# Performance work log

Measured on AMD Instinct MI355X. Metric: run time of the kernel, lower is better.

The kernel has to match this reference:

```python
import jax, jax.numpy as jnp
import numpy as np

HEADS = 8
DIM_HEAD = 64
WINDOW = 512
SCALE = DIM_HEAD ** -0.5


def setup_inputs() -> dict:
    key = jax.random.key(0)
    k1, k2, k3 = jax.random.split(key, 3)
    b, dim, n = 2, 256, 32768
    hidden = HEADS * DIM_HEAD  # 512
    x = jax.random.normal(k1, (b, dim, n), dtype=jnp.float32)
    # Conv1d(dim, hidden*3, 1, bias=False) weight -> [3*hidden, dim]
    w_qkv = jax.random.normal(k2, (3 * hidden, dim), dtype=jnp.float32) * (dim ** -0.5)
    # Conv1d(hidden, dim, 1) weight/bias
    w_out = jax.random.normal(k3, (dim, hidden), dtype=jnp.float32) * (hidden ** -0.5)
    b_out = jnp.zeros((dim,), dtype=jnp.float32)
    return {"x": x, "w_qkv": w_qkv, "w_out": w_out, "b_out": b_out}


def reference(x, w_qkv, w_out, b_out):
    b, c, n = x.shape
    h, d, w = HEADS, DIM_HEAD, WINDOW
    nw = n // w  # n chosen divisible by window size
    # 1x1 conv == channel matmul
    qkv = jnp.einsum('oc,bcn->bon', w_qkv, x)  # [b, 3*h*d, n]
    q, k, v = jnp.split(qkv, 3, axis=1)
    # [b, h, d, nw, w]
    def to_windows(t):
        return t.reshape(b, h, d, nw, w)
    q = to_windows(q) * SCALE
    k = to_windows(k)
    v = to_windows(v)
    # non-overlapping local windows: block-diagonal attention
    sim = jnp.einsum('bhdni,bhdnj->bhnij', q, k)        # [b,h,nw,w,w]
    attn = jax.nn.softmax(sim, axis=-1)
    out = jnp.einsum('bhnij,bhdnj->bhdni', attn, v)      # [b,h,d,nw,w]
    out = out.reshape(b, h * d, n)
    return jnp.einsum('oc,bcn->bon', w_out, out) + b_out[None, :, None]
```

## Files before the change

### kernel.cpp

```cpp
#include <hip/hip_runtime.h>
#include <stdint.h>
#include <stddef.h>


typedef _Float16 f16;
typedef _Float16 half8 __attribute__((ext_vector_type(8)));
typedef float f32x4 __attribute__((ext_vector_type(4)));

#define NSEQ 32768
#define NTOT 65536
#define WIN  512

__device__ __forceinline__ void async_copy16(const f16* g, f16* l) {
  __builtin_amdgcn_global_load_lds(
      (const __attribute__((address_space(1))) void*)g,
      (__attribute__((address_space(3))) void*)l, 16, 0, 0);
}

__device__ __forceinline__ int packrtz(float a, float b) {
  typedef __fp16 fp16v2 __attribute__((ext_vector_type(2)));
  fp16v2 h = __builtin_amdgcn_cvt_pkrtz(a, b);
  return __builtin_bit_cast(int, h);
}

__global__ __launch_bounds__(256) void convert_w(
    const float* __restrict__ wqkv, const float* __restrict__ wout,
    f16* __restrict__ wqh, f16* __restrict__ woh) {
  int idx = blockIdx.x * 256 + threadIdx.x;
  if (idx < 1536 * 256) {
    float v = wqkv[idx];
    if (idx < 512 * 256) v *= 0.125f;
    wqh[idx] = (f16)v;
  } else {
    int j = idx - 1536 * 256;
    if (j < 256 * 512) woh[j] = (f16)wout[j];
  }
}

__global__ __launch_bounds__(256) void transpose_x(
    const float* __restrict__ x, f16* __restrict__ xT) {
  __shared__ alignas(16) float tile[32][33];
  const int tx = threadIdx.x & 31, ty = threadIdx.x >> 5;
  const int bx = blockIdx.x, by = blockIdx.y;
  const float* xb = x + (size_t)blockIdx.z * 256 * NSEQ;
  f16* xTb = xT + (size_t)blockIdx.z * NSEQ * 256;
#pragma unroll
  for (int r = 0; r < 4; ++r) {
    int c = by * 32 + ty + r * 8;
    int n = bx * 32 + tx;
    tile[ty + r * 8][tx] = xb[(size_t)c * NSEQ + n];
  }
  __syncthreads();
#pragma unroll
  for (int r = 0; r < 4; ++r) {
    int n = bx * 32 + ty + r * 8;
    int c = by * 32 + tx;
    xTb[(size_t)n * 256 + c] = (f16)tile[tx][ty + r * 8];
  }
}

template <int MODE>
__global__ __launch_bounds__(256) void gemm_k(
    const f16* __restrict__ A, const f16* __restrict__ Bm,
    void* __restrict__ outp, const float* __restrict__ bias, int K,
    int bstride, int ostride) {
  __shared__ alignas(16) f16 As[8192];
  __shared__ alignas(16) f16 Bs[8192];
  const int tid = threadIdx.x;
  const int lane = tid & 63, wid = tid >> 6;
  const int quad = lane >> 4, lid = lane & 15;
  const int row0 = blockIdx.y * 128, col0 = blockIdx.x * 128;
  const int wm = (wid >> 1) * 64, wn = (wid & 1) * 64;

  f32x4 acc[4][4];
  const f32x4 zero = {0.f, 0.f, 0.f, 0.f};
#pragma unroll
  for (int i = 0; i < 4; ++i)
#pragma unroll
    for (int j = 0; j < 4; ++j) acc[i][j] = zero;

  const int kIters = K >> 6;
  for (int kt = 0; kt < kIters; ++kt) {
    __syncthreads();
    const int k0 = kt * 64;
#pragma unroll
    for (int rd = 0; rd < 4; ++rd) {
      int slot = rd * 256 + tid;
      int r = slot & 127, kc = slot >> 7;
      async_copy16(A + (size_t)(row0 + r) * K + k0 + kc * 8, As + slot * 8);
      async_copy16(Bm + (size_t)(col0 + r) * bstride + k0 + kc * 8,
                   Bs + slot * 8);
    }
    __syncthreads();

    half8 af[2][4], bf[2][4];
#pragma unroll
    for (int ks = 0; ks < 2; ++ks) {
#pragma unroll
      for (int mi = 0; mi < 4; ++mi)
        af[ks][mi] = *(const half8*)(As + ((ks * 4 + quad) * 128 + wm +
                                           mi * 16 + lid) * 8);
#pragma unroll
      for (int ni = 0; ni < 4; ++ni)
        bf[ks][ni] = *(const half8*)(Bs + ((ks * 4 + quad) * 128 + wn +
                                           ni * 16 + lid) * 8);
    }
#pragma unroll
    for (int ks = 0; ks < 2; ++ks)
#pragma unroll
      for (int mi = 0; mi < 4; ++mi)
#pragma unroll
        for (int ni = 0; ni < 4; ++ni)
          acc[mi][ni] = __builtin_amdgcn_mfma_f32_16x16x32_f16(
              af[ks][mi], bf[ks][ni], acc[mi][ni], 0, 0, 0);
  }

#pragma unroll
  for (int mi = 0; mi < 4; ++mi) {
#pragma unroll
    for (int r = 0; r < 4; ++r) {
      int grow = row0 + wm + mi * 16 + quad * 4 + r;
#pragma unroll
      for (int ni = 0; ni < 4; ++ni) {
        int gcol = col0 + wn + ni * 16 + lid;
        float v = acc[mi][ni][r];
        if (MODE == 2) {
          ((float*)outp)[(size_t)(gcol >> 15) * (256u * 32768u) +
                         (size_t)grow * 32768 + (gcol & 32767)] =
              v + bias[grow];
        } else {
          ((f16*)outp)[(size_t)grow * ostride + gcol] = (f16)v;
        }
      }
    }
  }
}

__global__ __launch_bounds__(512, 2) void attn_k(
    const f16* __restrict__ qk, const f16* __restrict__ vws,
    f16* __restrict__ ows) {
  __shared__ alignas(16) f16 smem[16384];

  const int tid = threadIdx.x;
  const int lane = tid & 63, wid = tid >> 6;
  const int quad = lane >> 4, lid = lane & 15;
  const int win = blockIdx.x;
  const int h = blockIdx.y;
  const size_t nbase = (size_t)blockIdx.z * NSEQ + (size_t)win * WIN;
  const int iw0 = wid * 64;

  half8 aq[4][2];
#pragma unroll
  for (int ig = 0; ig < 4; ++ig)
#pragma unroll
    for (int ks = 0; ks < 2; ++ks)
      aq[ig][ks] = *(const half8*)(qk + (nbase + iw0 + ig * 16 + lid) * 1024 +
                                   h * 64 + ks * 32 + quad * 8);

  f32x4 OT[4][4];
  const f32x4 zero = {0.f, 0.f, 0.f, 0.f};
#pragma unroll
  for (int di = 0; di < 4; ++di)
#pragma unroll
    for (int ig = 0; ig < 4; ++ig) OT[di][ig] = zero;
  float l_run[4] = {0.f, 0.f, 0.f, 0.f};

  const int sa = tid & 63, sc = tid >> 6;
  async_copy16(qk + (nbase + sa) * 1024 + 512 + h * 64 + sc * 8,
               smem + tid * 8);
  async_copy16(vws + (size_t)(h * 64 + sa) * NTOT + nbase + sc * 8,
               smem + 4096 + tid * 8);

  const int src0 = (quad & 1) * 32 + lid;
  const int src1 = src0 + 16;
  const bool hiq = quad >= 2;

  int p = 0;
  for (int jt = 0; jt < 8; ++jt) {
    __syncthreads();
    if (jt < 7) {
      const int j0n = (jt + 1) * 64;
      f16* Kb = smem + (1 - p) * 8192;
      async_copy16(qk + (nbase + j0n + sa) * 1024 + 512 + h * 64 + sc * 8,
                   Kb + tid * 8);
      async_copy16(vws + (size_t)(h * 64 + sa) * NTOT + nbase + j0n + sc * 8,
                   Kb + 4096 + tid * 8);
    }
    const f16* Ks = smem + p * 8192;
    const f16* Vs = smem + p * 8192 + 4096;

    f32x4 sT[4][4];
#pragma unroll
    for (int jg = 0; jg < 4; ++jg)
#pragma unroll
      for (int ig = 0; ig < 4; ++ig) sT[jg][ig] = zero;
#pragma unroll
    for (int ks = 0; ks < 2; ++ks)
#pragma unroll
      for (int jg = 0; jg < 4; ++jg) {
        half8 bk =
            *(const half8*)(Ks + ((ks * 4 + quad) * 64 + jg * 16 + lid) * 8);
#pragma unroll
        for (int ig = 0; ig < 4; ++ig)
          sT[jg][ig] = __builtin_amdgcn_mfma_f32_16x16x32_f16(
              bk, aq[ig][ks], sT[jg][ig], 0, 0, 0);
      }

    int pk[4][4][2];
#pragma unroll
    for (int jg = 0; jg < 4; ++jg)
#pragma unroll
      for (int ig = 0; ig < 4; ++ig) {
        float e0 = __expf(sT[jg][ig][0]);
        float e1 = __expf(sT[jg][ig][1]);
        float e2 = __expf(sT[jg][ig][2]);
        float e3 = __expf(sT[jg][ig][3]);
        l_run[ig] += (e0 + e1) + (e2 + e3);
        pk[jg][ig][0] = packrtz(e0, e1);
        pk[jg][ig][1] = packrtz(e2, e3);
      }

#pragma unroll
    for (int ks2 = 0; ks2 < 2; ++ks2) {
      half8 pt[4];
#pragma unroll
      for (int ig = 0; ig < 4; ++ig) {
        int w0a = __shfl(pk[ks2 * 2][ig][0], src0);
        int w0b = __shfl(pk[ks2 * 2 + 1][ig][0], src0);
        int w1a = __shfl(pk[ks2 * 2][ig][1], src0);
        int w1b = __shfl(pk[ks2 * 2 + 1][ig][1], src0);
        int w2a = __shfl(pk[ks2 * 2][ig][0], src1);
        int w2b = __shfl(pk[ks2 * 2 + 1][ig][0], src1);
        int w3a = __shfl(pk[ks2 * 2][ig][1], src1);
        int w3b = __shfl(pk[ks2 * 2 + 1][ig][1], src1);
        union {
          int i[4];
          half8 h;
        } u;
        u.i[0] = hiq ? w0b : w0a;
        u.i[1] = hiq ? w1b : w1a;
        u.i[2] = hiq ? w2b : w2a;
        u.i[3] = hiq ? w3b : w3a;
        pt[ig] = u.h;
      }
#pragma unroll
      for (int di = 0; di < 4; ++di) {
        half8 av =
            *(const half8*)(Vs + ((ks2 * 4 + quad) * 64 + di * 16 + lid) * 8);
#pragma unroll
        for (int ig = 0; ig < 4; ++ig)
          OT[di][ig] = __builtin_amdgcn_mfma_f32_16x16x32_f16(
              av, pt[ig], OT[di][ig], 0, 0, 0);
      }
    }
    p ^= 1;
  }

#pragma unroll
  for (int ig = 0; ig < 4; ++ig) {
    l_run[ig] += __shfl_xor(l_run[ig], 16, 64);
    l_run[ig] += __shfl_xor(l_run[ig], 32, 64);
  }

#pragma unroll
  for (int ig = 0; ig < 4; ++ig) {
    float inv = 1.0f / l_run[ig];
    size_t rowb = (nbase + iw0 + ig * 16 + lid) * 1024 + h * 64;
#pragma unroll
    for (int di = 0; di < 4; ++di) {
      int2 o;
      o.x = packrtz(OT[di][ig][0] * inv, OT[di][ig][1] * inv);
      o.y = packrtz(OT[di][ig][2] * inv, OT[di][ig][3] * inv);
      *(int2*)(ows + rowb + di * 16 + quad * 4) = o;
    }
  }
}

extern "C" void kernel_launch(void* const* d_in, const int* in_sizes, int n_in,
                              void* d_out, int out_size, void* d_ws,
                              size_t ws_size, hipStream_t stream) {
  const float* x = (const float*)d_in[0];
  const float* w_qkv = (const float*)d_in[1];
  const float* w_out = (const float*)d_in[2];
  const float* b_out = (const float*)d_in[3];

  char* ws = (char*)d_ws;
  f16* qkw = (f16*)(ws);
  f16* vw = (f16*)(ws + 134217728);
  f16* xT = (f16*)(ws + 201326592);
  f16* wqh = (f16*)(ws + 234881024);
  f16* woh = (f16*)(ws + 235667456);

  convert_w<<<2048, 256, 0, stream>>>(w_qkv, w_out, wqh, woh);
  transpose_x<<<dim3(1024, 8, 2), 256, 0, stream>>>(x, xT);
  gemm_k<0><<<dim3(8, 512), 256, 0, stream>>>(xT, wqh, qkw, nullptr, 256, 256,
                                              1024);
  gemm_k<0><<<dim3(512, 4), 256, 0, stream>>>(wqh + 1024 * 256, xT, vw,
                                              nullptr, 256, 256, NTOT);
  attn_k<<<dim3(64, 8, 2), 512, 0, stream>>>(qkw, vw, qkw);
  gemm_k<2><<<dim3(512, 2), 256, 0, stream>>>(woh, qkw, d_out, b_out, 512,
                                              1024, 0);
}
```

Before: 433.5 us.

## Load K/V fragments directly from global into registers, drop LDS staging

```diff
diff --git a/kernel.cpp b/kernel.cpp
--- a/kernel.cpp
+++ b/kernel.cpp
@@ -10,6 +10,7 @@
 #define NSEQ 32768
 #define NTOT 65536
 #define WIN  512
+#define QSCALE 0.18033688011112042f
 
 __device__ __forceinline__ void async_copy16(const f16* g, f16* l) {
   __builtin_amdgcn_global_load_lds(
@@ -29,7 +30,7 @@
   int idx = blockIdx.x * 256 + threadIdx.x;
   if (idx < 1536 * 256) {
     float v = wqkv[idx];
-    if (idx < 512 * 256) v *= 0.125f;
+    if (idx < 512 * 256) v *= QSCALE;
     wqh[idx] = (f16)v;
   } else {
     int j = idx - 1536 * 256;
@@ -136,26 +137,29 @@
   }
 }
 
-__global__ __launch_bounds__(512, 2) void attn_k(
+__global__ __launch_bounds__(256) void attn_k(
     const f16* __restrict__ qk, const f16* __restrict__ vws,
     f16* __restrict__ ows) {
-  __shared__ alignas(16) f16 smem[16384];
-
   const int tid = threadIdx.x;
   const int lane = tid & 63, wid = tid >> 6;
   const int quad = lane >> 4, lid = lane & 15;
-  const int win = blockIdx.x;
-  const int h = blockIdx.y;
-  const size_t nbase = (size_t)blockIdx.z * NSEQ + (size_t)win * WIN;
-  const int iw0 = wid * 64;
+  const int ih = blockIdx.x;
+  const int win = blockIdx.y;
+  const int h = blockIdx.z & 7, b = blockIdx.z >> 3;
+  const size_t nbase = (size_t)b * NSEQ + (size_t)win * WIN;
+  const int iw0 = ih * 256 + wid * 64;
+
+  const f16* qbase = qk + nbase * 1024 + h * 64;
+  const f16* kbase = qk + nbase * 1024 + 512 + h * 64;
+  const f16* vbase = vws + (size_t)(h * 64) * NTOT + nbase;
 
   half8 aq[4][2];
 #pragma unroll
   for (int ig = 0; ig < 4; ++ig)
 #pragma unroll
     for (int ks = 0; ks < 2; ++ks)
-      aq[ig][ks] = *(const half8*)(qk + (nbase + iw0 + ig * 16 + lid) * 1024 +
-                                   h * 64 + ks * 32 + quad * 8);
+      aq[ig][ks] = *(const half8*)(qbase + (size_t)(iw0 + ig * 16 + lid) * 1024 +
+                                   ks * 32 + quad * 8);
 
   f32x4 OT[4][4];
   const f32x4 zero = {0.f, 0.f, 0.f, 0.f};
@@ -164,30 +168,30 @@
 #pragma unroll
     for (int ig = 0; ig < 4; ++ig) OT[di][ig] = zero;
   float l_run[4] = {0.f, 0.f, 0.f, 0.f};
-
-  const int sa = tid & 63, sc = tid >> 6;
-  async_copy16(qk + (nbase + sa) * 1024 + 512 + h * 64 + sc * 8,
-               smem + tid * 8);
-  async_copy16(vws + (size_t)(h * 64 + sa) * NTOT + nbase + sc * 8,
-               smem + 4096 + tid * 8);
 
   const int src0 = (quad & 1) * 32 + lid;
   const int src1 = src0 + 16;
   const bool hiq = quad >= 2;
 
-  int p = 0;
   for (int jt = 0; jt < 8; ++jt) {
-    __syncthreads();
-    if (jt < 7) {
-      const int j0n = (jt + 1) * 64;
-      f16* Kb = smem + (1 - p) * 8192;
-      async_copy16(qk + (nbase + j0n + sa) * 1024 + 512 + h * 64 + sc * 8,
-                   Kb + tid * 8);
-      async_copy16(vws + (size_t)(h * 64 + sa) * NTOT + nbase + j0n + sc * 8,
-                   Kb + 4096 + tid * 8);
-    }
-    const f16* Ks = smem + p * 8192;
-    const f16* Vs = smem + p * 8192 + 4096;
+    const int j0 = jt * 64;
+
+    half8 kf[2][4];
+#pragma unroll
+    for (int ks = 0; ks < 2; ++ks)
+#pragma unroll
+      for (int jg = 0; jg < 4; ++jg)
+        kf[ks][jg] =
+            *(const half8*)(kbase + (size_t)(j0 + jg * 16 + lid) * 1024 +
+                            ks * 32 + quad * 8);
+    half8 vf[2][4];
+#pragma unroll
+    for (int ks2 = 0; ks2 < 2; ++ks2)
+#pragma unroll
+      for (int di = 0; di < 4; ++di)
+        vf[ks2][di] =
+            *(const half8*)(vbase + (size_t)(di * 16 + lid) * NTOT + j0 +
+                            ks2 * 32 + quad * 8);
 
     f32x4 sT[4][4];
 #pragma unroll
@@ -197,24 +201,21 @@
 #pragma unroll
     for (int ks = 0; ks < 2; ++ks)
 #pragma unroll
-      for (int jg = 0; jg < 4; ++jg) {
-        half8 bk =
-            *(const half8*)(Ks + ((ks * 4 + quad) * 64 + jg * 16 + lid) * 8);
+      for (int jg = 0; jg < 4; ++jg)
 #pragma unroll
         for (int ig = 0; ig < 4; ++ig)
           sT[jg][ig] = __builtin_amdgcn_mfma_f32_16x16x32_f16(
-              bk, aq[ig][ks], sT[jg][ig], 0, 0, 0);
-      }
+              kf[ks][jg], aq[ig][ks], sT[jg][ig], 0, 0, 0);
 
     int pk[4][4][2];
 #pragma unroll
     for (int jg = 0; jg < 4; ++jg)
 #pragma unroll
       for (int ig = 0; ig < 4; ++ig) {
-        float e0 = __expf(sT[jg][ig][0]);
-        float e1 = __expf(sT[jg][ig][1]);
-        float e2 = __expf(sT[jg][ig][2]);
-        float e3 = __expf(sT[jg][ig][3]);
+        float e0 = exp2f(sT[jg][ig][0]);
+        float e1 = exp2f(sT[jg][ig][1]);
+        float e2 = exp2f(sT[jg][ig][2]);
+        float e3 = exp2f(sT[jg][ig][3]);
         l_run[ig] += (e0 + e1) + (e2 + e3);
         pk[jg][ig][0] = packrtz(e0, e1);
         pk[jg][ig][1] = packrtz(e2, e3);
@@ -244,16 +245,12 @@
         pt[ig] = u.h;
       }
 #pragma unroll
-      for (int di = 0; di < 4; ++di) {
-        half8 av =
-            *(const half8*)(Vs + ((ks2 * 4 + quad) * 64 + di * 16 + lid) * 8);
+      for (int di = 0; di < 4; ++di)
 #pragma unroll
         for (int ig = 0; ig < 4; ++ig)
           OT[di][ig] = __builtin_amdgcn_mfma_f32_16x16x32_f16(
-              av, pt[ig], OT[di][ig], 0, 0, 0);
-      }
-    }
-    p ^= 1;
+              vf[ks2][di], pt[ig], OT[di][ig], 0, 0, 0);
+    }
   }
 
 #pragma unroll
@@ -297,7 +294,7 @@
                                               1024);
   gemm_k<0><<<dim3(512, 4), 256, 0, stream>>>(wqh + 1024 * 256, xT, vw,
                                               nullptr, 256, 256, NTOT);
-  attn_k<<<dim3(64, 8, 2), 512, 0, stream>>>(qkw, vw, qkw);
+  attn_k<<<dim3(2, 64, 16), 256, 0, stream>>>(qkw, vw, qkw);
   gemm_k<2><<<dim3(512, 2), 256, 0, stream>>>(woh, qkw, d_out, b_out, 512,
                                               1024, 0);
 }
```

After: 555.7 us. +28.2%, slower.
